# Performance work log

Hardware: AMD Instinct MI355X
Metric: run time of the kernel (lower is better)

## Reference

```python
import jax, jax.numpy as jnp
import numpy as np

N_NODES = 100000
DROP_P = 0.2


def _degree_norm(idx, n):
    deg = jax.ops.segment_sum(jnp.ones_like(idx, dtype=jnp.float32), idx, num_segments=n)
    return jnp.maximum(deg, 1.0) ** -0.5


def gcn_layer(x, src, dst, W, b, n):
    # DGL GraphConv, norm='both', in_feats > out_feats so weight is applied first.
    norm_src = _degree_norm(src, n)  # out-degree^{-1/2}
    norm_dst = _degree_norm(dst, n)  # in-degree^{-1/2}
    h = (x * norm_src[:, None]) @ W            # [N, d_out]
    agg = jax.ops.segment_sum(h[src], dst, num_segments=n)  # gather-scatter over edges
    return agg * norm_dst[:, None] + b


def setup_inputs() -> dict:
    key = jax.random.key(0)
    k = jax.random.split(key, 5)
    x = jax.random.normal(k[0], (N_NODES, 256), dtype=jnp.float32)
    edge_index = jax.random.randint(k[1], (2, 1600000), 0, N_NODES, dtype=jnp.int64)
    W1 = jax.random.normal(k[2], (256, 128), dtype=jnp.float32) * (1.0 / np.sqrt(256))
    b1 = jnp.zeros((128,), dtype=jnp.float32)
    W2 = jax.random.normal(k[3], (128, 47), dtype=jnp.float32) * (1.0 / np.sqrt(128))
    b2 = jnp.zeros((47,), dtype=jnp.float32)
    return {"x": x, "edge_index": edge_index, "W1": W1, "b1": b1, "W2": W2, "b2": b2}


def reference(x, edge_index, W1, b1, W2, b2):
    src, dst = edge_index[0], edge_index[1]
    n = x.shape[0]
    # CRD: GraphConv -> relu -> dropout (F.dropout default training=True; fixed mask)
    h = gcn_layer(x, src, dst, W1, b1, n)
    h = jax.nn.relu(h)
    keep = jax.random.bernoulli(jax.random.key(42), 1.0 - DROP_P, h.shape)
    h = jnp.where(keep, h / (1.0 - DROP_P), 0.0)
    # CLS: GraphConv -> log_softmax over class dim
    out = gcn_layer(h, src, dst, W2, b2, n)
    return jax.nn.log_softmax(out, axis=-1)
```

## Files before the change

### kernel.cpp

```cpp
#include <hip/hip_runtime.h>
#include <math.h>


#define NF0 256
#define NF1 128
#define NC  47
#define CB  1024

typedef __attribute__((ext_vector_type(8))) short bfrag;
typedef __attribute__((ext_vector_type(4))) float f32x4;

__device__ __forceinline__ unsigned short f2bf(float f) {
  unsigned u = __float_as_uint(f);
  return (unsigned short)((u + 0x7fffu + ((u >> 16) & 1u)) >> 16);
}
__device__ __forceinline__ unsigned pack2bf(float a, float b) {
  return (unsigned)f2bf(a) | ((unsigned)f2bf(b) << 16);
}
__device__ __forceinline__ float bflo(unsigned v) { return __uint_as_float(v << 16); }
__device__ __forceinline__ float bfhi(unsigned v) { return __uint_as_float(v & 0xffff0000u); }
__device__ __forceinline__ float bf2f(unsigned short b) {
  return __uint_as_float((unsigned)b << 16);
}

__device__ __forceinline__ unsigned rotl_(unsigned x, int n) {
  return (x << n) | (x >> (32 - n));
}
__device__ __forceinline__ void threefry2x32_(unsigned x0, unsigned x1,
                                              unsigned& o0, unsigned& o1) {
  const unsigned k0 = 0u, k1 = 42u;
  const unsigned k2 = k0 ^ k1 ^ 0x1BD11BDAu;
  x0 += k0; x1 += k1;
  x0+=x1; x1=rotl_(x1,13); x1^=x0;
  x0+=x1; x1=rotl_(x1,15); x1^=x0;
  x0+=x1; x1=rotl_(x1,26); x1^=x0;
  x0+=x1; x1=rotl_(x1, 6); x1^=x0;
  x0+=k1; x1+=k2+1u;
  x0+=x1; x1=rotl_(x1,17); x1^=x0;
  x0+=x1; x1=rotl_(x1,29); x1^=x0;
  x0+=x1; x1=rotl_(x1,16); x1^=x0;
  x0+=x1; x1=rotl_(x1,24); x1^=x0;
  x0+=k2; x1+=k0+2u;
  x0+=x1; x1=rotl_(x1,13); x1^=x0;
  x0+=x1; x1=rotl_(x1,15); x1^=x0;
  x0+=x1; x1=rotl_(x1,26); x1^=x0;
  x0+=x1; x1=rotl_(x1, 6); x1^=x0;
  x0+=k0; x1+=k1+3u;
  x0+=x1; x1=rotl_(x1,17); x1^=x0;
  x0+=x1; x1=rotl_(x1,29); x1^=x0;
  x0+=x1; x1=rotl_(x1,16); x1^=x0;
  x0+=x1; x1=rotl_(x1,24); x1^=x0;
  x0+=k1; x1+=k2+4u;
  x0+=x1; x1=rotl_(x1,13); x1^=x0;
  x0+=x1; x1=rotl_(x1,15); x1^=x0;
  x0+=x1; x1=rotl_(x1,26); x1^=x0;
  x0+=x1; x1=rotl_(x1, 6); x1^=x0;
  x0+=k2; x1+=k0+5u;
  o0 = x0; o1 = x1;
}
__device__ __forceinline__ float dropout_mul(int j) {
  unsigned o0, o1;
  threefry2x32_(0u, (unsigned)j, o0, o1);
  unsigned bits = o0 ^ o1;
  float u = __uint_as_float((bits >> 9) | 0x3f800000u) - 1.0f;
  return (u < 0.8f) ? 1.25f : 0.0f;
}


__global__ __launch_bounds__(256) void k_chist(const int* __restrict__ ei, int E,
                                               int nbk,
                                               unsigned* __restrict__ bCntD,
                                               unsigned* __restrict__ bCntS,
                                               const float* __restrict__ W1,
                                               const float* __restrict__ W2,
                                               unsigned* __restrict__ W1t32,
                                               unsigned* __restrict__ W2t32) {
  if (blockIdx.x >= 256) {
    int i = (blockIdx.x - 256) * 256 + threadIdx.x;
    if (i < 128 * 128) {
      int n = i >> 7, k = (i & 127) << 1;
      W1t32[i] = pack2bf(W1[(size_t)k * NF1 + n], W1[(size_t)(k + 1) * NF1 + n]);
    } else if (i < 128 * 128 + 48 * 64) {
      int j = i - 128 * 128;
      int f = j >> 6, k = (j & 63) << 1;
      float a = (f < NC) ? W2[(size_t)k * NC + f] : 0.f;
      float c = (f < NC) ? W2[(size_t)(k + 1) * NC + f] : 0.f;
      W2t32[j] = pack2bf(a, c);
    }
    return;
  }
  __shared__ unsigned hd[128], hs[128];
  for (int i = threadIdx.x; i < 128; i += 256) { hd[i] = 0; hs[i] = 0; }
  __syncthreads();
  for (int e = blockIdx.x * 256 + threadIdx.x; e < E; e += 256 * 256) {
    int s = ei[e], d = ei[E + e];
    atomicAdd(&hs[s >> 10], 1u);
    atomicAdd(&hd[d >> 10], 1u);
  }
  __syncthreads();
  for (int i = threadIdx.x; i < nbk; i += 256) {
    if (hd[i]) atomicAdd(&bCntD[i], hd[i]);
    if (hs[i]) atomicAdd(&bCntS[i], hs[i]);
  }
}

__global__ __launch_bounds__(256) void k_cscatter(const int* __restrict__ ei, int E,
                                                  const unsigned* __restrict__ bCntD,
                                                  const unsigned* __restrict__ bCntS,
                                                  unsigned* __restrict__ curD,
                                                  unsigned* __restrict__ curS,
                                                  unsigned* __restrict__ pd,
                                                  unsigned short* __restrict__ ps,
                                                  int nbk) {
  __shared__ unsigned hd[128], hs[128];
  __shared__ unsigned baseD[128], baseS[128];
  __shared__ unsigned sc[256];
  const int t = threadIdx.x;
  int per = (E + gridDim.x - 1) / gridDim.x;
  int e0 = blockIdx.x * per;
  int e1 = min(e0 + per, E);
  unsigned orig = (t < 128) ? ((t < nbk) ? bCntD[t] : 0u)
                            : (((t - 128) < nbk) ? bCntS[t - 128] : 0u);
  sc[t] = orig;
  if (t < 128) { hd[t] = 0; hs[t] = 0; }
  __syncthreads();
  for (int e = e0 + t; e < e1; e += 256) {
    int s = ei[e], d = ei[E + e];
    atomicAdd(&hs[s >> 10], 1u);
    atomicAdd(&hd[d >> 10], 1u);
  }
  __syncthreads();
  #pragma unroll
  for (int o = 1; o < 128; o <<= 1) {
    unsigned u = ((t & 127) >= o) ? sc[t - o] : 0u;
    __syncthreads();
    sc[t] += u;
    __syncthreads();
  }
  if (t < 128) {
    unsigned excl = sc[t] - orig;
    unsigned h = hd[t];
    baseD[t] = excl + (h ? atomicAdd(&curD[t], h) : 0u);
    hd[t] = 0;
  } else {
    int i = t - 128;
    unsigned excl = sc[t] - orig;
    unsigned h = hs[i];
    baseS[i] = excl + (h ? atomicAdd(&curS[i], h) : 0u);
    hs[i] = 0;
  }
  __syncthreads();
  for (int e = e0 + t; e < e1; e += 256) {
    int s = ei[e], d = ei[E + e];
    int bd = d >> 10, bs = s >> 10;
    unsigned pD = baseD[bd] + atomicAdd(&hd[bd], 1u);
    unsigned pS = baseS[bs] + atomicAdd(&hs[bs], 1u);
    pd[pD] = ((unsigned)(d & (CB - 1)) << 17) | (unsigned)s;
    ps[pS] = (unsigned short)(s & (CB - 1));
  }
}

__global__ __launch_bounds__(256) void k_fine(const unsigned* __restrict__ bCntD,
                                              const unsigned* __restrict__ bCntS,
                                              const unsigned* __restrict__ pd,
                                              const unsigned short* __restrict__ ps,
                                              unsigned* __restrict__ off,
                                              float* __restrict__ norm_dst,
                                              float* __restrict__ norm_src,
                                              int* __restrict__ csr,
                                              int N, int E, int nbk) {
  __shared__ unsigned cnt[CB];
  __shared__ unsigned part[256];
  __shared__ unsigned sc[256];
  const int t = threadIdx.x;
  const bool isD = (int)blockIdx.x < nbk;
  const int b = isD ? (int)blockIdx.x : ((int)blockIdx.x - nbk);
  unsigned orig = (t < 128) ? ((t < nbk) ? bCntD[t] : 0u)
                            : (((t - 128) < nbk) ? bCntS[t - 128] : 0u);
  sc[t] = orig;
  __syncthreads();
  #pragma unroll
  for (int o = 1; o < 128; o <<= 1) {
    unsigned u = ((t & 127) >= o) ? sc[t - o] : 0u;
    __syncthreads();
    sc[t] += u;
    __syncthreads();
  }
  const int idx = isD ? b : (128 + b);
  const unsigned hi = sc[idx];
  const unsigned lo = hi - (isD ? bCntD[b] : bCntS[b]);
  const int base = b << 10;
  for (int i = t; i < CB; i += 256) cnt[i] = 0;
  __syncthreads();
  if (isD) {
    for (unsigned j = lo + t; j < hi; j += 256) atomicAdd(&cnt[pd[j] >> 17], 1u);
    __syncthreads();
    unsigned c0 = cnt[4*t], c1 = cnt[4*t+1], c2 = cnt[4*t+2], c3 = cnt[4*t+3];
    unsigned tsum = c0 + c1 + c2 + c3;
    part[t] = tsum;
    __syncthreads();
    #pragma unroll
    for (int o = 1; o < 256; o <<= 1) {
      unsigned u = (t >= o) ? part[t - o] : 0u;
      __syncthreads();
      part[t] += u;
      __syncthreads();
    }
    unsigned e0 = part[t] - tsum;
    unsigned p0 = e0, p1 = e0 + c0, p2 = p1 + c1, p3 = p2 + c2;
    int n0 = base + 4 * t;
    if (n0 + 0 < N) { off[n0+0] = lo + p0; norm_dst[n0+0] = 1.0f / sqrtf((float)(c0 < 1u ? 1u : c0)); }
    if (n0 + 1 < N) { off[n0+1] = lo + p1; norm_dst[n0+1] = 1.0f / sqrtf((float)(c1 < 1u ? 1u : c1)); }
    if (n0 + 2 < N) { off[n0+2] = lo + p2; norm_dst[n0+2] = 1.0f / sqrtf((float)(c2 < 1u ? 1u : c2)); }
    if (n0 + 3 < N) { off[n0+3] = lo + p3; norm_dst[n0+3] = 1.0f / sqrtf((float)(c3 < 1u ? 1u : c3)); }
    if (b == nbk - 1 && t == 0) off[N] = (unsigned)E;
    __syncthreads();
    cnt[4*t] = p0; cnt[4*t+1] = p1; cnt[4*t+2] = p2; cnt[4*t+3] = p3;
    __syncthreads();
    for (unsigned j = lo + t; j < hi; j += 256) {
      unsigned v = pd[j];
      unsigned pos = atomicAdd(&cnt[v >> 17], 1u);
      csr[lo + pos] = (int)(v & 0x1FFFFu);
    }
  } else {
    for (unsigned j = lo + t; j < hi; j += 256) atomicAdd(&cnt[ps[j]], 1u);
    __syncthreads();
    for (int i = t; i < CB; i += 256) {
      int n = base + i;
      if (n < N) {
        unsigned c = cnt[i];
        norm_src[n] = 1.0f / sqrtf((float)(c < 1u ? 1u : c));
      }
    }
  }
}

__global__ __launch_bounds__(256) void k_gemm1(const float* __restrict__ x,
                                               const unsigned* __restrict__ W1t32,
                                               const float* __restrict__ norm_src,
                                               unsigned short* __restrict__ h1, int N) {
  __shared__ unsigned As[128][20];
  __shared__ unsigned Bs[128][20];
  const int m0 = blockIdx.x * 128;
  const int t = threadIdx.x;
  const int lane = t & 63, wid = t >> 6;
  const int fr = lane & 15, ko = (lane >> 4) * 8;

  f32x4 acc[2][8];
  #pragma unroll
  for (int r = 0; r < 2; r++)
    #pragma unroll
    for (int c = 0; c < 8; c++) acc[r][c] = (f32x4){0.f, 0.f, 0.f, 0.f};

  const int sr = t >> 1;
  const int shw = (t & 1) * 8;

  for (int k0 = 0; k0 < NF0; k0 += 32) {
    {
      unsigned w[8];
      int gm = m0 + sr;
      if (gm < N) {
        const float* p = x + (size_t)gm * NF0 + k0 + shw * 2;
        #pragma unroll
        for (int q = 0; q < 4; q++) {
          float4 v = *(const float4*)(p + q * 4);
          w[2*q]   = pack2bf(v.x, v.y);
          w[2*q+1] = pack2bf(v.z, v.w);
        }
      } else {
        #pragma unroll
        for (int q = 0; q < 8; q++) w[q] = 0u;
      }
      *(uint4*)&As[sr][shw]     = make_uint4(w[0], w[1], w[2], w[3]);
      *(uint4*)&As[sr][shw + 4] = make_uint4(w[4], w[5], w[6], w[7]);
    }
    {
      const unsigned* pb = W1t32 + (size_t)sr * (NF0 / 2) + (k0 >> 1) + shw;
      *(uint4*)&Bs[sr][shw]     = *(const uint4*)pb;
      *(uint4*)&Bs[sr][shw + 4] = *(const uint4*)(pb + 4);
    }
    __syncthreads();
    const unsigned short* As16 = (const unsigned short*)&As[0][0];
    const unsigned short* Bs16 = (const unsigned short*)&Bs[0][0];
    #pragma unroll
    for (int r = 0; r < 2; r++) {
      bfrag a = *(const bfrag*)(As16 + (size_t)(wid * 32 + r * 16 + fr) * 40 + ko);
      #pragma unroll
      for (int c = 0; c < 8; c++) {
        bfrag b = *(const bfrag*)(Bs16 + (size_t)(c * 16 + fr) * 40 + ko);
        acc[r][c] = __builtin_amdgcn_mfma_f32_16x16x32_bf16(a, b, acc[r][c], 0, 0, 0);
      }
    }
    __syncthreads();
  }

  #pragma unroll
  for (int r = 0; r < 2; r++) {
    int rbase = m0 + wid * 32 + r * 16 + (lane >> 4) * 4;
    float ns[4];
    #pragma unroll
    for (int g = 0; g < 4; g++) ns[g] = (rbase + g < N) ? norm_src[rbase + g] : 0.f;
    #pragma unroll
    for (int c = 0; c < 8; c++) {
      int col = c * 16 + fr;
      #pragma unroll
      for (int g = 0; g < 4; g++) {
        int row = rbase + g;
        if (row < N) h1[(size_t)row * NF1 + col] = f2bf(acc[r][c][g] * ns[g]);
      }
    }
  }
}

#define W2STR 66
__global__ __launch_bounds__(256) void k_g1g2(const unsigned* __restrict__ off,
                                              const int* __restrict__ csr,
                                              const unsigned short* __restrict__ h1,
                                              const float* __restrict__ norm_dst,
                                              const float* __restrict__ norm_src,
                                              const float* __restrict__ b1,
                                              const unsigned* __restrict__ W2t32,
                                              unsigned short* __restrict__ g, int N) {
  __shared__ unsigned W2L[48 * W2STR];
  __shared__ unsigned row[4 * 64];
  const int t = threadIdx.x;
  const int lane = t & 63, wid = t >> 6;
  for (int i = t; i < 48 * 64; i += 256) {
    W2L[(i >> 6) * W2STR + (i & 63)] = W2t32[i];
  }
  __syncthreads();

  const int f = lane << 1;
  unsigned* rp = &row[wid * 64];
  const unsigned* wp = &W2L[lane * W2STR];
  const int ngroups = (N + 3) >> 2;

  for (int grp = blockIdx.x; grp < ngroups; grp += gridDim.x) {
    int node = grp * 4 + wid;
    if (node >= N) continue;
    unsigned j = off[node], e1 = off[node + 1];
    float ax = 0.f, ay = 0.f;
    for (; j + 4 <= e1; j += 4) {
      int s0 = csr[j], s1 = csr[j+1], s2 = csr[j+2], s3 = csr[j+3];
      unsigned v0 = *(const unsigned*)(h1 + (size_t)s0 * NF1 + f);
      unsigned v1 = *(const unsigned*)(h1 + (size_t)s1 * NF1 + f);
      unsigned v2 = *(const unsigned*)(h1 + (size_t)s2 * NF1 + f);
      unsigned v3 = *(const unsigned*)(h1 + (size_t)s3 * NF1 + f);
      ax += (bflo(v0) + bflo(v1)) + (bflo(v2) + bflo(v3));
      ay += (bfhi(v0) + bfhi(v1)) + (bfhi(v2) + bfhi(v3));
    }
    for (; j < e1; j++) {
      unsigned v = *(const unsigned*)(h1 + (size_t)csr[j] * NF1 + f);
      ax += bflo(v); ay += bfhi(v);
    }
    float nd = norm_dst[node], ns = norm_src[node];
    float2 bb = *(const float2*)(b1 + f);
    float v0 = fmaxf(ax * nd + bb.x, 0.f);
    float v1 = fmaxf(ay * nd + bb.y, 0.f);
    int jf = node * NF1 + f;
    v0 *= dropout_mul(jf) * ns;
    v1 *= dropout_mul(jf + 1) * ns;
    rp[lane] = pack2bf(v0, v1);
    __builtin_amdgcn_wave_barrier();
    if (lane < 48) {
      float acc = 0.f;
      #pragma unroll
      for (int kp = 0; kp < 64; kp += 2) {
        uint2 u = *(const uint2*)(rp + kp);
        uint2 w = *(const uint2*)(wp + kp);
        acc += bflo(u.x) * bflo(w.x) + bfhi(u.x) * bfhi(w.x)
             + bflo(u.y) * bflo(w.y) + bfhi(u.y) * bfhi(w.y);
      }
      g[(size_t)node * 48 + lane] = f2bf(acc);
    }
    __builtin_amdgcn_wave_barrier();
  }
}

__global__ __launch_bounds__(256) void k_gather2(const unsigned* __restrict__ off,
                                                 const int* __restrict__ csr,
                                                 const unsigned short* __restrict__ g,
                                                 const float* __restrict__ norm_dst,
                                                 const float* __restrict__ b2,
                                                 float* __restrict__ out, int N) {
  int node = (blockIdx.x * 256 + threadIdx.x) >> 6;
  int lane = threadIdx.x & 63;
  if (node >= N) return;
  unsigned j = off[node], e1 = off[node + 1];
  float acc = 0.f;
  for (; j + 4 <= e1; j += 4) {
    int s0 = csr[j], s1 = csr[j+1], s2 = csr[j+2], s3 = csr[j+3];
    if (lane < 48) {
      float a0 = bf2f(g[(size_t)s0 * 48 + lane]);
      float a1 = bf2f(g[(size_t)s1 * 48 + lane]);
      float a2 = bf2f(g[(size_t)s2 * 48 + lane]);
      float a3 = bf2f(g[(size_t)s3 * 48 + lane]);
      acc += (a0 + a1) + (a2 + a3);
    }
  }
  for (; j < e1; j++) {
    if (lane < 48) acc += bf2f(g[(size_t)csr[j] * 48 + lane]);
  }
  float nd = norm_dst[node];
  float vr = 0.f, m = -INFINITY;
  if (lane < NC) {
    vr = acc * nd + b2[lane];
    m = vr;
  }
  #pragma unroll
  for (int o = 32; o; o >>= 1) m = fmaxf(m, __shfl_xor(m, o));
  float ex = (lane < NC) ? expf(vr - m) : 0.f;
  #pragma unroll
  for (int o = 32; o; o >>= 1) ex += __shfl_xor(ex, o);
  float ls = logf(ex);
  if (lane < NC) out[(size_t)node * NC + lane] = vr - m - ls;
}

extern "C" void kernel_launch(void* const* d_in, const int* in_sizes, int n_in,
                              void* d_out, int out_size, void* d_ws, size_t ws_size,
                              hipStream_t stream) {
  const float* x  = (const float*)d_in[0];
  const int*   ei = (const int*)d_in[1];
  const float* W1 = (const float*)d_in[2];
  const float* b1 = (const float*)d_in[3];
  const float* W2 = (const float*)d_in[4];
  const float* b2 = (const float*)d_in[5];
  float* out = (float*)d_out;

  const int N = in_sizes[0] / NF0;
  const int E = in_sizes[1] / 2;
  const int nbk = (N + CB - 1) / CB;

  unsigned* ws = (unsigned*)d_ws;
  size_t o = 0;
  auto alloc = [&](size_t elems) { size_t p = o; o += (elems + 3) & ~(size_t)3; return p; };
  float*    norm_src = (float*)(ws + alloc(N));
  float*    norm_dst = (float*)(ws + alloc(N));
  unsigned* off      = ws + alloc(N + 1);
  unsigned* bCntD    = ws + alloc(128);
  unsigned* bCntS    = ws + alloc(128);
  unsigned* curD     = ws + alloc(128);
  unsigned* curS     = ws + alloc(128);
  unsigned* pd       = ws + alloc(E);
  unsigned short* ps = (unsigned short*)(ws + alloc(E / 2));
  int*      csr      = (int*)(ws + alloc(E));
  unsigned* W1t32    = ws + alloc(128 * 128);
  unsigned* W2t32    = ws + alloc(48 * 64);
  unsigned short* h1 = (unsigned short*)(ws + alloc((size_t)N * NF1 / 2));
  unsigned short* gbuf;
  if ((size_t)E * 3 >= (size_t)N * 48) {
    gbuf = (unsigned short*)pd;
  } else {
    gbuf = (unsigned short*)(ws + alloc(((size_t)N * 48 + 1) / 2));
  }

  hipMemsetAsync(bCntD, 0, 512 * sizeof(unsigned), stream);

  int wblk = (128 * 128 + 48 * 64 + 255) / 256;
  k_chist<<<256 + wblk, 256, 0, stream>>>(ei, E, nbk, bCntD, bCntS, W1, W2, W1t32, W2t32);
  k_cscatter<<<256, 256, 0, stream>>>(ei, E, bCntD, bCntS, curD, curS, pd, ps, nbk);
  k_fine<<<2 * nbk, 256, 0, stream>>>(bCntD, bCntS, pd, ps, off, norm_dst, norm_src,
                                      csr, N, E, nbk);
  k_gemm1<<<(N + 127) / 128, 256, 0, stream>>>(x, W1t32, norm_src, h1, N);
  k_g1g2<<<2048, 256, 0, stream>>>(off, csr, h1, norm_dst, norm_src, b1,
                                   W2t32, gbuf, N);
  k_gather2<<<((size_t)N * 64 + 255) / 256, 256, 0, stream>>>(
      off, csr, gbuf, norm_dst, b2, out, N);
}
```

Measured before the change: 494.3 us.

## Batch 64 aggregated rows per block and compute layer-2 projection with MFMA

The fused gather+W2 kernel now lets each wave aggregate 16 nodes into a shared-memory tile, then runs the 128x48 projection with bf16 MFMA 16x16x32 instructions instead of a per-node scalar dot product on 48 lanes. The grid becomes one block per 64 nodes rather than a 2048-block grid-stride loop. This removes the scalar FMA work and per-node LDS reads in the projection. It costs more shared memory per block (hrows tile), which can lower occupancy for the latency-bound gather.

```diff
diff --git a/kernel.cpp b/kernel.cpp
--- a/kernel.cpp
+++ b/kernel.cpp
@@ -312,7 +312,7 @@
   }
 }
 
-#define W2STR 66
+#define HSTR 68
 __global__ __launch_bounds__(256) void k_g1g2(const unsigned* __restrict__ off,
                                               const int* __restrict__ csr,
                                               const unsigned short* __restrict__ h1,
@@ -321,23 +321,23 @@
                                               const float* __restrict__ b1,
                                               const unsigned* __restrict__ W2t32,
                                               unsigned short* __restrict__ g, int N) {
-  __shared__ unsigned W2L[48 * W2STR];
-  __shared__ unsigned row[4 * 64];
+  __shared__ unsigned W2L[48 * HSTR];
+  __shared__ unsigned hrows[64 * HSTR];
   const int t = threadIdx.x;
   const int lane = t & 63, wid = t >> 6;
-  for (int i = t; i < 48 * 64; i += 256) {
-    W2L[(i >> 6) * W2STR + (i & 63)] = W2t32[i];
-  }
+  for (int i = t; i < 48 * 64; i += 256)
+    W2L[(i >> 6) * HSTR + (i & 63)] = W2t32[i];
   __syncthreads();
 
   const int f = lane << 1;
-  unsigned* rp = &row[wid * 64];
-  const unsigned* wp = &W2L[lane * W2STR];
-  const int ngroups = (N + 3) >> 2;
-
-  for (int grp = blockIdx.x; grp < ngroups; grp += gridDim.x) {
-    int node = grp * 4 + wid;
-    if (node >= N) continue;
+  const int fr = lane & 15, hi4 = lane >> 4;
+  const int base = blockIdx.x * 64;
+
+  #pragma unroll 1
+  for (int i = 0; i < 16; i++) {
+    const int node = base + wid * 16 + i;
+    unsigned* rp = &hrows[(wid * 16 + i) * HSTR];
+    if (node >= N) { rp[lane] = 0u; continue; }
     unsigned j = off[node], e1 = off[node + 1];
     float ax = 0.f, ay = 0.f;
     for (; j + 4 <= e1; j += 4) {
@@ -361,19 +361,35 @@
     v0 *= dropout_mul(jf) * ns;
     v1 *= dropout_mul(jf + 1) * ns;
     rp[lane] = pack2bf(v0, v1);
-    __builtin_amdgcn_wave_barrier();
-    if (lane < 48) {
-      float acc = 0.f;
-      #pragma unroll
-      for (int kp = 0; kp < 64; kp += 2) {
-        uint2 u = *(const uint2*)(rp + kp);
-        uint2 w = *(const uint2*)(wp + kp);
-        acc += bflo(u.x) * bflo(w.x) + bfhi(u.x) * bfhi(w.x)
-             + bflo(u.y) * bflo(w.y) + bfhi(u.y) * bfhi(w.y);
-      }
-      g[(size_t)node * 48 + lane] = f2bf(acc);
-    }
-    __builtin_amdgcn_wave_barrier();
+  }
+  __builtin_amdgcn_wave_barrier();
+  __asm__ volatile("" ::: "memory");
+
+  const unsigned short* H16 = (const unsigned short*)hrows;
+  const unsigned short* B16 = (const unsigned short*)W2L;
+  bfrag a[4];
+  #pragma unroll
+  for (int kk = 0; kk < 4; kk++)
+    a[kk] = *(const bfrag*)(H16 + (size_t)(wid * 16 + fr) * (2 * HSTR) + kk * 32 + hi4 * 8);
+  f32x4 acc[3];
+  #pragma unroll
+  for (int c = 0; c < 3; c++) {
+    acc[c] = (f32x4){0.f, 0.f, 0.f, 0.f};
+    #pragma unroll
+    for (int kk = 0; kk < 4; kk++) {
+      bfrag b = *(const bfrag*)(B16 + (size_t)(c * 16 + fr) * (2 * HSTR) + kk * 32 + hi4 * 8);
+      acc[c] = __builtin_amdgcn_mfma_f32_16x16x32_bf16(a[kk], b, acc[c], 0, 0, 0);
+    }
+  }
+  const int rbase = base + wid * 16 + hi4 * 4;
+  #pragma unroll
+  for (int c = 0; c < 3; c++) {
+    int col = c * 16 + fr;
+    #pragma unroll
+    for (int r = 0; r < 4; r++) {
+      int nr = rbase + r;
+      if (nr < N) g[(size_t)nr * 48 + col] = f2bf(acc[c][r]);
+    }
   }
 }
 
@@ -462,8 +478,8 @@
   k_fine<<<2 * nbk, 256, 0, stream>>>(bCntD, bCntS, pd, ps, off, norm_dst, norm_src,
                                       csr, N, E, nbk);
   k_gemm1<<<(N + 127) / 128, 256, 0, stream>>>(x, W1t32, norm_src, h1, N);
-  k_g1g2<<<2048, 256, 0, stream>>>(off, csr, h1, norm_dst, norm_src, b1,
-                                   W2t32, gbuf, N);
+  k_g1g2<<<(N + 63) / 64, 256, 0, stream>>>(off, csr, h1, norm_dst, norm_src, b1,
+                                            W2t32, gbuf, N);
   k_gather2<<<((size_t)N * 64 + 255) / 256, 256, 0, stream>>>(
       off, csr, gbuf, norm_dst, b2, out, N);
 }
```

After: 509.8 us. 3.1% more time.

## Split fused gather+GEMM2 into gather kernel and separate MFMA GEMM kernel

Applied to the files above, without the earlier changes.

The fused per-node gather with a scalar LDS dot product for the second weight multiply is split into two kernels. The first writes the activated, dropout-scaled bf16 hidden rows to an intermediate buffer, and the second runs the 128x48 projection with bf16 MFMA instructions. This removes the per-node scalar dot-product loop and its wave barriers, but adds an extra kernel launch and a global write and read of the N x 128 bf16 intermediate. Padding rows in the intermediate are left uninitialized, though their outputs are masked.

```diff
diff --git a/kernel.cpp b/kernel.cpp
--- a/kernel.cpp
+++ b/kernel.cpp
@@ -312,28 +312,18 @@
   }
 }
 
-#define W2STR 66
-__global__ __launch_bounds__(256) void k_g1g2(const unsigned* __restrict__ off,
-                                              const int* __restrict__ csr,
-                                              const unsigned short* __restrict__ h1,
-                                              const float* __restrict__ norm_dst,
-                                              const float* __restrict__ norm_src,
-                                              const float* __restrict__ b1,
-                                              const unsigned* __restrict__ W2t32,
-                                              unsigned short* __restrict__ g, int N) {
-  __shared__ unsigned W2L[48 * W2STR];
-  __shared__ unsigned row[4 * 64];
+__global__ __launch_bounds__(256) void k_gather1(const unsigned* __restrict__ off,
+                                                 const int* __restrict__ csr,
+                                                 const unsigned short* __restrict__ h1,
+                                                 const float* __restrict__ norm_dst,
+                                                 const float* __restrict__ norm_src,
+                                                 const float* __restrict__ b1,
+                                                 unsigned* __restrict__ h2, int N) {
   const int t = threadIdx.x;
   const int lane = t & 63, wid = t >> 6;
-  for (int i = t; i < 48 * 64; i += 256) {
-    W2L[(i >> 6) * W2STR + (i & 63)] = W2t32[i];
-  }
-  __syncthreads();
-
   const int f = lane << 1;
-  unsigned* rp = &row[wid * 64];
-  const unsigned* wp = &W2L[lane * W2STR];
   const int ngroups = (N + 3) >> 2;
+  const float2 bb = *(const float2*)(b1 + f);
 
   for (int grp = blockIdx.x; grp < ngroups; grp += gridDim.x) {
     int node = grp * 4 + wid;
@@ -354,26 +344,48 @@
       ax += bflo(v); ay += bfhi(v);
     }
     float nd = norm_dst[node], ns = norm_src[node];
-    float2 bb = *(const float2*)(b1 + f);
     float v0 = fmaxf(ax * nd + bb.x, 0.f);
     float v1 = fmaxf(ay * nd + bb.y, 0.f);
     int jf = node * NF1 + f;
     v0 *= dropout_mul(jf) * ns;
     v1 *= dropout_mul(jf + 1) * ns;
-    rp[lane] = pack2bf(v0, v1);
-    __builtin_amdgcn_wave_barrier();
-    if (lane < 48) {
-      float acc = 0.f;
-      #pragma unroll
-      for (int kp = 0; kp < 64; kp += 2) {
-        uint2 u = *(const uint2*)(rp + kp);
-        uint2 w = *(const uint2*)(wp + kp);
-        acc += bflo(u.x) * bflo(w.x) + bfhi(u.x) * bfhi(w.x)
-             + bflo(u.y) * bflo(w.y) + bfhi(u.y) * bfhi(w.y);
-      }
-      g[(size_t)node * 48 + lane] = f2bf(acc);
-    }
-    __builtin_amdgcn_wave_barrier();
+    h2[(size_t)node * 64 + lane] = pack2bf(v0, v1);
+  }
+}
+
+__global__ __launch_bounds__(256) void k_gemm2(const unsigned* __restrict__ h2,
+                                               const unsigned* __restrict__ W2t32,
+                                               unsigned short* __restrict__ g, int N) {
+  const int t = threadIdx.x;
+  const int lane = t & 63, wid = t >> 6;
+  const int fr = lane & 15, hi4 = lane >> 4;
+  const int row = blockIdx.x * 64 + wid * 16 + fr;
+
+  bfrag a[4];
+  const unsigned* ap = h2 + (size_t)row * 64 + hi4 * 4;
+  #pragma unroll
+  for (int kk = 0; kk < 4; kk++) {
+    uint4 v = *(const uint4*)(ap + kk * 16);
+    a[kk] = *(bfrag*)&v;
+  }
+
+  const int rbase = blockIdx.x * 64 + wid * 16 + hi4 * 4;
+  #pragma unroll
+  for (int c = 0; c < 3; c++) {
+    f32x4 acc = (f32x4){0.f, 0.f, 0.f, 0.f};
+    const unsigned* bp = W2t32 + (size_t)(c * 16 + fr) * 64 + hi4 * 4;
+    #pragma unroll
+    for (int kk = 0; kk < 4; kk++) {
+      uint4 w = *(const uint4*)(bp + kk * 16);
+      bfrag b = *(bfrag*)&w;
+      acc = __builtin_amdgcn_mfma_f32_16x16x32_bf16(a[kk], b, acc, 0, 0, 0);
+    }
+    int col = c * 16 + fr;
+    #pragma unroll
+    for (int r = 0; r < 4; r++) {
+      int nr = rbase + r;
+      if (nr < N) g[(size_t)nr * 48 + col] = f2bf(acc[r]);
+    }
   }
 }
 
@@ -430,6 +442,7 @@
   const int N = in_sizes[0] / NF0;
   const int E = in_sizes[1] / 2;
   const int nbk = (N + CB - 1) / CB;
+  const int Npad = (N + 63) & ~63;
 
   unsigned* ws = (unsigned*)d_ws;
   size_t o = 0;
@@ -447,6 +460,7 @@
   unsigned* W1t32    = ws + alloc(128 * 128);
   unsigned* W2t32    = ws + alloc(48 * 64);
   unsigned short* h1 = (unsigned short*)(ws + alloc((size_t)N * NF1 / 2));
+  unsigned* h2       = ws + alloc((size_t)Npad * 64);
   unsigned short* gbuf;
   if ((size_t)E * 3 >= (size_t)N * 48) {
     gbuf = (unsigned short*)pd;
@@ -462,8 +476,8 @@
   k_fine<<<2 * nbk, 256, 0, stream>>>(bCntD, bCntS, pd, ps, off, norm_dst, norm_src,
                                       csr, N, E, nbk);
   k_gemm1<<<(N + 127) / 128, 256, 0, stream>>>(x, W1t32, norm_src, h1, N);
-  k_g1g2<<<2048, 256, 0, stream>>>(off, csr, h1, norm_dst, norm_src, b1,
-                                   W2t32, gbuf, N);
+  k_gather1<<<2048, 256, 0, stream>>>(off, csr, h1, norm_dst, norm_src, b1, h2, N);
+  k_gemm2<<<Npad / 64, 256, 0, stream>>>(h2, W2t32, gbuf, N);
   k_gather2<<<((size_t)N * 64 + 255) / 256, 256, 0, stream>>>(
       off, csr, gbuf, norm_dst, b2, out, N);
 }
```

Measured after the change: 466.9 us. 1.06x faster.
